# Kernel optimization log

Measured on AMD Instinct MI355X. Metric: run time of the kernel, lower is better.

## Reference

```python
import jax, jax.numpy as jnp
import numpy as np
from jax import lax


def build_scharr_filter(size):
    assert size % 2 == 1
    c = size // 2
    wx = np.zeros((size, size), np.float32)
    wy = np.zeros((size, size), np.float32)
    for i in range(size):
        for j in range(size):
            dx = j - c
            dy = i - c
            wx[i, j] = dx * (3 if abs(dx) == 1 else 10 if dx == 0 else 1)
            wy[i, j] = dy * (3 if abs(dy) == 1 else 10 if dy == 0 else 1)
    return jnp.asarray(wx), jnp.asarray(wy)


SIZE = 3


def build_normals(xyz, size=SIZE):
    # xyz: (B, 3, H, W). Depthwise conv: for each of x,y,z apply scharr_x and scharr_y.
    kx, ky = build_scharr_filter(size)
    # kernel (6,1,s,s): [Sxx, Sxy, Syx, Syy, Szx, Szy] via feature_group_count=3
    kernel = jnp.stack([kx, ky, kx, ky, kx, ky])[:, None]
    p = size // 2
    g = lax.conv_general_dilated(
        xyz, kernel, window_strides=(1, 1), padding=[(p, p), (p, p)],
        dimension_numbers=("NCHW", "OIHW", "NCHW"), feature_group_count=3)
    Sxx, Sxy = g[:, 0:1], g[:, 1:2]
    Syx, Syy = g[:, 2:3], g[:, 3:4]
    Szx, Szy = g[:, 4:5], g[:, 5:6]
    normal = jnp.concatenate([
        Syx * Szy - Szx * Syy,
        Szx * Sxy - Szy * Sxx,
        Sxx * Syy - Syx * Sxy,
    ], axis=1)
    n = jnp.linalg.norm(normal, axis=1, keepdims=True) + jnp.float32(1e-10)
    return normal / n


def setup_inputs() -> dict:
    key = jax.random.key(0)
    k1, k2, k3 = jax.random.split(key, 3)
    B, H, W = 16, 384, 1280
    xyz_pred = jax.random.normal(k1, (B, 3, H, W), dtype=jnp.float32)
    xyz_gt = jax.random.normal(k2, (B, 3, H, W), dtype=jnp.float32)
    mask = jax.random.uniform(k3, (B, 1, H, W), dtype=jnp.float32)
    return {"xyz_pred": xyz_pred, "xyz_gt": xyz_gt, "mask": mask}


def reference(xyz_pred, xyz_gt, mask):
    normals_pred = build_normals(xyz_pred)
    normals_gt = build_normals(xyz_gt)
    loss = jnp.sum(mask * jnp.abs(normals_pred - normals_gt))
    denom = jnp.sum(mask)
    return loss / denom
```

## Files before the change

### kernel.cpp

```cpp
#include <hip/hip_runtime.h>

#define BB  16
#define HH  384
#define WW  1280
#define ROWS 16
#define CPW 62
#define NGROUP 21
#define NSLOT 64


__device__ __forceinline__ float load_col(const float* __restrict__ plane,
                                          int i, int j, bool jok) {
    return jok ? plane[(size_t)i * WW + j] : 0.f;
}

__device__ __forceinline__ void taps(float v, float& D, float& T) {
    const float lft = __shfl_up(v, 1, 64);
    const float rgt = __shfl_down(v, 1, 64);
    D = rgt - lft;
    T = lft + v + rgt;
}

__device__ __forceinline__ float normal_absdiff(const float* gx, const float* gy)
{
    float n0p = gx[1] * gy[2] - gx[2] * gy[1];
    float n1p = gx[2] * gy[0] - gx[0] * gy[2];
    float n2p = gx[0] * gy[1] - gx[1] * gy[0];
    float n0g = gx[4] * gy[5] - gx[5] * gy[4];
    float n1g = gx[5] * gy[3] - gx[3] * gy[5];
    float n2g = gx[3] * gy[4] - gx[4] * gy[3];
    float sp = n0p * n0p + n1p * n1p + n2p * n2p;
    float sg = n0g * n0g + n1g * n1g + n2g * n2g;
    float ip = (sp > 1e-20f) ? __builtin_amdgcn_rsqf(sp) : 0.f;
    float ig = (sg > 1e-20f) ? __builtin_amdgcn_rsqf(sg) : 0.f;
    return fabsf(n0p * ip - n0g * ig) + fabsf(n1p * ip - n1g * ig)
         + fabsf(n2p * ip - n2g * ig);
}

__global__ __launch_bounds__(64)
void NormalLoss_44478681317469_main(const float* __restrict__ pred,
                                    const float* __restrict__ gt,
                                    const float* __restrict__ mask,
                                    double* __restrict__ acc)
{
    const int lane = threadIdx.x;
    const int j    = blockIdx.x * CPW - 1 + lane;
    const bool jok = (unsigned)j < WW;
    const int r0   = blockIdx.y * ROWS;
    const int b    = blockIdx.z;
    const bool out_ok = (lane >= 1) && (lane <= CPW) && jok;

    const float* pl[6];
#pragma unroll
    for (int c = 0; c < 3; ++c) {
        pl[c]     = pred + (size_t)(b * 3 + c) * HH * WW;
        pl[3 + c] = gt   + (size_t)(b * 3 + c) * HH * WW;
    }
    const float* mpl = mask + (size_t)b * HH * WW;

    float Dm1[6], D0[6], Tm1[6], T0[6];
    float Rv[6];

#pragma unroll
    for (int c = 0; c < 6; ++c) {
        if (r0 > 0) {
            float v = load_col(pl[c], r0 - 1, j, jok);
            taps(v, Dm1[c], Tm1[c]);
        } else { Dm1[c] = 0.f; Tm1[c] = 0.f; }
        {
            float v = load_col(pl[c], r0, j, jok);
            taps(v, D0[c], T0[c]);
        }
    }

#pragma unroll
    for (int c = 0; c < 6; ++c)
        Rv[c] = load_col(pl[c], r0 + 1, j, jok);
    float mrow = jok ? mpl[(size_t)r0 * WW + j] : 0.f;

    float lsum = 0.f, msum = 0.f;

#pragma unroll 2
    for (int k = 0; k < ROWS; ++k) {
        const int i = r0 + k;

        float Dp1[6], Tp1[6];
#pragma unroll
        for (int c = 0; c < 6; ++c) taps(Rv[c], Dp1[c], Tp1[c]);
        const float m = out_ok ? mrow : 0.f;

        if (i + 2 < HH) {
#pragma unroll
            for (int c = 0; c < 6; ++c) Rv[c] = load_col(pl[c], i + 2, j, jok);
        } else {
#pragma unroll
            for (int c = 0; c < 6; ++c) Rv[c] = 0.f;
        }
        if (k + 1 < ROWS) mrow = jok ? mpl[(size_t)(i + 1) * WW + j] : 0.f;

        float gx[6], gy[6];
#pragma unroll
        for (int c = 0; c < 6; ++c) {
            gx[c] = Dm1[c] + D0[c] + Dp1[c];
            gy[c] = Tp1[c] - Tm1[c];
        }

        const float d = normal_absdiff(gx, gy);
        lsum += m * d;
        msum += m;

#pragma unroll
        for (int c = 0; c < 6; ++c) {
            Dm1[c] = D0[c]; D0[c] = Dp1[c];
            Tm1[c] = T0[c]; T0[c] = Tp1[c];
        }
    }

#pragma unroll
    for (int off = 32; off > 0; off >>= 1) {
        lsum += __shfl_down(lsum, off, 64);
        msum += __shfl_down(msum, off, 64);
    }
    if (lane == 0) {
        const int linear = (blockIdx.z * gridDim.y + blockIdx.y) * gridDim.x + blockIdx.x;
        double* slot = acc + (size_t)(linear & (NSLOT - 1)) * 8;
        atomicAdd(&slot[0], (double)lsum);
        atomicAdd(&slot[1], (double)msum);
    }
}

__global__ void NormalLoss_44478681317469_final(const double* __restrict__ acc,
                                                float* __restrict__ out)
{
    const int t = threadIdx.x;
    double L = acc[(size_t)t * 8 + 0];
    double M = acc[(size_t)t * 8 + 1];
#pragma unroll
    for (int off = 32; off > 0; off >>= 1) {
        L += __shfl_down(L, off, 64);
        M += __shfl_down(M, off, 64);
    }
    if (t == 0) out[0] = (float)(L / M);
}

extern "C" void kernel_launch(void* const* d_in, const int* in_sizes, int n_in,
                              void* d_out, int out_size, void* d_ws, size_t ws_size,
                              hipStream_t stream)
{
    const float* pred = (const float*)d_in[0];
    const float* gt   = (const float*)d_in[1];
    const float* mask = (const float*)d_in[2];
    double* acc = (double*)d_ws;

    hipMemsetAsync(acc, 0, NSLOT * 8 * sizeof(double), stream);

    dim3 grid(NGROUP, HH / ROWS, BB);
    NormalLoss_44478681317469_main<<<grid, dim3(64), 0, stream>>>(pred, gt, mask, acc);
    NormalLoss_44478681317469_final<<<1, 64, 0, stream>>>(acc, (float*)d_out);
}
```

Baseline: 242.7 us.

## Process two columns per lane with float2 loads and edge halo fetch

Each lane now handles two adjacent columns through float2 loads, so a 64-lane wave covers 128 output columns instead of 62. The old layout wasted two halo lanes per wave; now only the end lanes issue an extra scalar load for the halo. This cuts redundant loads and shuffles per output and widens memory transactions. The cost is roughly double the register state per lane, which may lower occupancy.

```diff
diff --git a/kernel.cpp b/kernel.cpp
--- a/kernel.cpp
+++ b/kernel.cpp
@@ -1,24 +1,32 @@
 #include <hip/hip_runtime.h>
+
 
 #define BB  16
 #define HH  384
 #define WW  1280
 #define ROWS 16
-#define CPW 62
-#define NGROUP 21
+#define CPW 128
 #define NSLOT 64
 
 
-__device__ __forceinline__ float load_col(const float* __restrict__ plane,
-                                          int i, int j, bool jok) {
-    return jok ? plane[(size_t)i * WW + j] : 0.f;
+__device__ __forceinline__ void fetch_pair_edge(const float* __restrict__ plane,
+                                                int i, int x0, int ej, bool eok,
+                                                float& a, float& b, float& e) {
+    const float* row = plane + (size_t)i * WW;
+    const float2 ab = *reinterpret_cast<const float2*>(row + x0);
+    a = ab.x; b = ab.y;
+    e = eok ? row[ej] : 0.f;
 }
 
-__device__ __forceinline__ void taps(float v, float& D, float& T) {
-    const float lft = __shfl_up(v, 1, 64);
-    const float rgt = __shfl_down(v, 1, 64);
-    D = rgt - lft;
-    T = lft + v + rgt;
+__device__ __forceinline__ void htaps(float a, float b, float e, int lane,
+                                      float& Da, float& Db, float& Ta, float& Tb) {
+    float l = __shfl_up(b, 1, 64);
+    float r = __shfl_down(a, 1, 64);
+    if (lane == 0)  l = e;
+    if (lane == 63) r = e;
+    const float s = a + b;
+    Da = b - l;  Db = r - a;
+    Ta = l + s;  Tb = s + r;
 }
 
 __device__ __forceinline__ float normal_absdiff(const float* gx, const float* gy)
@@ -44,11 +52,13 @@
                                     double* __restrict__ acc)
 {
     const int lane = threadIdx.x;
-    const int j    = blockIdx.x * CPW - 1 + lane;
-    const bool jok = (unsigned)j < WW;
+    const int S    = blockIdx.x * CPW;
+    const int x0   = S + 2 * lane;
     const int r0   = blockIdx.y * ROWS;
     const int b    = blockIdx.z;
-    const bool out_ok = (lane >= 1) && (lane <= CPW) && jok;
+
+    const int  ej  = (lane == 0) ? (x0 - 1) : (x0 + 2);
+    const bool eok = ((lane == 0) || (lane == 63)) && ((unsigned)ej < WW);
 
     const float* pl[6];
 #pragma unroll
@@ -58,25 +68,26 @@
     }
     const float* mpl = mask + (size_t)b * HH * WW;
 
-    float Dm1[6], D0[6], Tm1[6], T0[6];
-    float Rv[6];
+    float Dm1a[6], Dm1b[6], D0a[6], D0b[6];
+    float Tm1a[6], Tm1b[6], T0a[6], T0b[6];
+    float Ra[6], Rb[6], Re[6];
 
 #pragma unroll
     for (int c = 0; c < 6; ++c) {
         if (r0 > 0) {
-            float v = load_col(pl[c], r0 - 1, j, jok);
-            taps(v, Dm1[c], Tm1[c]);
-        } else { Dm1[c] = 0.f; Tm1[c] = 0.f; }
+            float a, bb, e; fetch_pair_edge(pl[c], r0 - 1, x0, ej, eok, a, bb, e);
+            htaps(a, bb, e, lane, Dm1a[c], Dm1b[c], Tm1a[c], Tm1b[c]);
+        } else { Dm1a[c] = 0.f; Dm1b[c] = 0.f; Tm1a[c] = 0.f; Tm1b[c] = 0.f; }
         {
-            float v = load_col(pl[c], r0, j, jok);
-            taps(v, D0[c], T0[c]);
+            float a, bb, e; fetch_pair_edge(pl[c], r0, x0, ej, eok, a, bb, e);
+            htaps(a, bb, e, lane, D0a[c], D0b[c], T0a[c], T0b[c]);
         }
     }
 
 #pragma unroll
     for (int c = 0; c < 6; ++c)
-        Rv[c] = load_col(pl[c], r0 + 1, j, jok);
-    float mrow = jok ? mpl[(size_t)r0 * WW + j] : 0.f;
+        fetch_pair_edge(pl[c], r0 + 1, x0, ej, eok, Ra[c], Rb[c], Re[c]);
+    float2 mrow = *reinterpret_cast<const float2*>(mpl + (size_t)r0 * WW + x0);
 
     float lsum = 0.f, msum = 0.f;
 
@@ -84,35 +95,43 @@
     for (int k = 0; k < ROWS; ++k) {
         const int i = r0 + k;
 
-        float Dp1[6], Tp1[6];
+        float Dp1a[6], Dp1b[6], Tp1a[6], Tp1b[6];
 #pragma unroll
-        for (int c = 0; c < 6; ++c) taps(Rv[c], Dp1[c], Tp1[c]);
-        const float m = out_ok ? mrow : 0.f;
+        for (int c = 0; c < 6; ++c)
+            htaps(Ra[c], Rb[c], Re[c], lane, Dp1a[c], Dp1b[c], Tp1a[c], Tp1b[c]);
+        const float2 m = mrow;
 
         if (i + 2 < HH) {
 #pragma unroll
-            for (int c = 0; c < 6; ++c) Rv[c] = load_col(pl[c], i + 2, j, jok);
+            for (int c = 0; c < 6; ++c)
+                fetch_pair_edge(pl[c], i + 2, x0, ej, eok, Ra[c], Rb[c], Re[c]);
         } else {
 #pragma unroll
-            for (int c = 0; c < 6; ++c) Rv[c] = 0.f;
+            for (int c = 0; c < 6; ++c) { Ra[c] = 0.f; Rb[c] = 0.f; Re[c] = 0.f; }
         }
-        if (k + 1 < ROWS) mrow = jok ? mpl[(size_t)(i + 1) * WW + j] : 0.f;
+        if (k + 1 < ROWS)
+            mrow = *reinterpret_cast<const float2*>(mpl + (size_t)(i + 1) * WW + x0);
 
-        float gx[6], gy[6];
+        float gxa[6], gxb[6], gya[6], gyb[6];
 #pragma unroll
         for (int c = 0; c < 6; ++c) {
-            gx[c] = Dm1[c] + D0[c] + Dp1[c];
-            gy[c] = Tp1[c] - Tm1[c];
+            gxa[c] = Dm1a[c] + D0a[c] + Dp1a[c];
+            gxb[c] = Dm1b[c] + D0b[c] + Dp1b[c];
+            gya[c] = Tp1a[c] - Tm1a[c];
+            gyb[c] = Tp1b[c] - Tm1b[c];
         }
 
-        const float d = normal_absdiff(gx, gy);
-        lsum += m * d;
-        msum += m;
+        const float da = normal_absdiff(gxa, gya);
+        const float db = normal_absdiff(gxb, gyb);
+        lsum += m.x * da + m.y * db;
+        msum += m.x + m.y;
 
 #pragma unroll
         for (int c = 0; c < 6; ++c) {
-            Dm1[c] = D0[c]; D0[c] = Dp1[c];
-            Tm1[c] = T0[c]; T0[c] = Tp1[c];
+            Dm1a[c] = D0a[c]; D0a[c] = Dp1a[c];
+            Dm1b[c] = D0b[c]; D0b[c] = Dp1b[c];
+            Tm1a[c] = T0a[c]; T0a[c] = Tp1a[c];
+            Tm1b[c] = T0b[c]; T0b[c] = Tp1b[c];
         }
     }
 
@@ -154,7 +173,7 @@
 
     hipMemsetAsync(acc, 0, NSLOT * 8 * sizeof(double), stream);
 
-    dim3 grid(NGROUP, HH / ROWS, BB);
+    dim3 grid(WW / CPW, HH / ROWS, BB);
     NormalLoss_44478681317469_main<<<grid, dim3(64), 0, stream>>>(pred, gt, mask, acc);
     NormalLoss_44478681317469_final<<<1, 64, 0, stream>>>(acc, (float*)d_out);
 }
```

Measured after the change: 249.7 us. 1.03x slower.

## Process four columns per lane with float4 loads and no halo lanes

Applied to the files above, without the earlier changes.

Each lane now handles four adjacent columns, loaded as one float4, so a 64-lane wave covers 256 columns. Edge lanes fetch one extra scalar halo value instead of a whole wave reserving two halo lanes. This removes the duplicated halo loads and idle lanes, cuts the number of shuffles per output, and widens the memory accesses. It costs more registers for the per-column rolling state and shrinks the grid to five blocks across the width, which lowers parallelism per row band.

```diff
diff --git a/kernel.cpp b/kernel.cpp
--- a/kernel.cpp
+++ b/kernel.cpp
@@ -4,21 +4,26 @@
 #define HH  384
 #define WW  1280
 #define ROWS 16
-#define CPW 62
-#define NGROUP 21
+#define CPW 256
 #define NSLOT 64
 
 
-__device__ __forceinline__ float load_col(const float* __restrict__ plane,
-                                          int i, int j, bool jok) {
-    return jok ? plane[(size_t)i * WW + j] : 0.f;
+__device__ __forceinline__ void load_q(const float* __restrict__ plane, int i, int x0,
+                                       int ej, bool eok, float4& v, float& e) {
+    const float* row = plane + (size_t)i * WW;
+    v = *reinterpret_cast<const float4*>(row + x0);
+    e = eok ? row[ej] : 0.f;
 }
 
-__device__ __forceinline__ void taps(float v, float& D, float& T) {
-    const float lft = __shfl_up(v, 1, 64);
-    const float rgt = __shfl_down(v, 1, 64);
-    D = rgt - lft;
-    T = lft + v + rgt;
+__device__ __forceinline__ void taps4(const float4 v, float e, int lane,
+                                      float D[4], float T[4]) {
+    float l = __shfl_up(v.w, 1, 64);
+    float r = __shfl_down(v.x, 1, 64);
+    if (lane == 0)  l = e;
+    if (lane == 63) r = e;
+    const float s01 = v.x + v.y, s23 = v.z + v.w;
+    D[0] = v.y - l;   D[1] = v.z - v.x;   D[2] = v.w - v.y;   D[3] = r - v.z;
+    T[0] = l + s01;   T[1] = s01 + v.z;   T[2] = v.y + s23;   T[3] = s23 + r;
 }
 
 __device__ __forceinline__ float normal_absdiff(const float* gx, const float* gy)
@@ -44,11 +49,13 @@
                                     double* __restrict__ acc)
 {
     const int lane = threadIdx.x;
-    const int j    = blockIdx.x * CPW - 1 + lane;
-    const bool jok = (unsigned)j < WW;
+    const int S    = blockIdx.x * CPW;
+    const int x0   = S + 4 * lane;
     const int r0   = blockIdx.y * ROWS;
     const int b    = blockIdx.z;
-    const bool out_ok = (lane >= 1) && (lane <= CPW) && jok;
+
+    const int  ej  = (lane == 0) ? (x0 - 1) : (x0 + 4);
+    const bool eok = ((lane == 0) || (lane == 63)) && ((unsigned)ej < WW);
 
     const float* pl[6];
 #pragma unroll
@@ -58,62 +65,75 @@
     }
     const float* mpl = mask + (size_t)b * HH * WW;
 
-    float Dm1[6], D0[6], Tm1[6], T0[6];
-    float Rv[6];
+    float Dm1[6][4], D0[6][4], Tm1[6][4], T0[6][4];
+    float4 Rv[6]; float Re[6];
 
 #pragma unroll
     for (int c = 0; c < 6; ++c) {
         if (r0 > 0) {
-            float v = load_col(pl[c], r0 - 1, j, jok);
-            taps(v, Dm1[c], Tm1[c]);
-        } else { Dm1[c] = 0.f; Tm1[c] = 0.f; }
+            float4 v; float e; load_q(pl[c], r0 - 1, x0, ej, eok, v, e);
+            taps4(v, e, lane, Dm1[c], Tm1[c]);
+        } else {
+#pragma unroll
+            for (int q = 0; q < 4; ++q) { Dm1[c][q] = 0.f; Tm1[c][q] = 0.f; }
+        }
         {
-            float v = load_col(pl[c], r0, j, jok);
-            taps(v, D0[c], T0[c]);
+            float4 v; float e; load_q(pl[c], r0, x0, ej, eok, v, e);
+            taps4(v, e, lane, D0[c], T0[c]);
         }
     }
 
 #pragma unroll
     for (int c = 0; c < 6; ++c)
-        Rv[c] = load_col(pl[c], r0 + 1, j, jok);
-    float mrow = jok ? mpl[(size_t)r0 * WW + j] : 0.f;
+        load_q(pl[c], r0 + 1, x0, ej, eok, Rv[c], Re[c]);
+    float4 mrow = *reinterpret_cast<const float4*>(mpl + (size_t)r0 * WW + x0);
 
     float lsum = 0.f, msum = 0.f;
 
-#pragma unroll 2
     for (int k = 0; k < ROWS; ++k) {
         const int i = r0 + k;
 
-        float Dp1[6], Tp1[6];
+        float lR[6], rR[6];
 #pragma unroll
-        for (int c = 0; c < 6; ++c) taps(Rv[c], Dp1[c], Tp1[c]);
-        const float m = out_ok ? mrow : 0.f;
+        for (int c = 0; c < 6; ++c) {
+            float l = __shfl_up(Rv[c].w, 1, 64);
+            float r = __shfl_down(Rv[c].x, 1, 64);
+            if (lane == 0)  l = Re[c];
+            if (lane == 63) r = Re[c];
+            lR[c] = l; rR[c] = r;
+        }
+        const float4 m = mrow;
+
+#pragma unroll
+        for (int q = 0; q < 4; ++q) {
+            float gx[6], gy[6];
+#pragma unroll
+            for (int c = 0; c < 6; ++c) {
+                const float4 R = Rv[c];
+                float Dp1, Tp1;
+                if (q == 0)      { Dp1 = R.y - lR[c];  Tp1 = lR[c] + R.x + R.y; }
+                else if (q == 1) { Dp1 = R.z - R.x;    Tp1 = R.x + R.y + R.z; }
+                else if (q == 2) { Dp1 = R.w - R.y;    Tp1 = R.y + R.z + R.w; }
+                else             { Dp1 = rR[c] - R.z;  Tp1 = R.z + R.w + rR[c]; }
+                gx[c] = Dm1[c][q] + D0[c][q] + Dp1;
+                gy[c] = Tp1 - Tm1[c][q];
+                Dm1[c][q] = D0[c][q]; D0[c][q] = Dp1;
+                Tm1[c][q] = T0[c][q]; T0[c][q] = Tp1;
+            }
+            const float mq = (q == 0) ? m.x : (q == 1) ? m.y : (q == 2) ? m.z : m.w;
+            lsum += mq * normal_absdiff(gx, gy);
+            msum += mq;
+        }
 
         if (i + 2 < HH) {
 #pragma unroll
-            for (int c = 0; c < 6; ++c) Rv[c] = load_col(pl[c], i + 2, j, jok);
+            for (int c = 0; c < 6; ++c) load_q(pl[c], i + 2, x0, ej, eok, Rv[c], Re[c]);
         } else {
 #pragma unroll
-            for (int c = 0; c < 6; ++c) Rv[c] = 0.f;
+            for (int c = 0; c < 6; ++c) { Rv[c] = make_float4(0.f, 0.f, 0.f, 0.f); Re[c] = 0.f; }
         }
-        if (k + 1 < ROWS) mrow = jok ? mpl[(size_t)(i + 1) * WW + j] : 0.f;
-
-        float gx[6], gy[6];
-#pragma unroll
-        for (int c = 0; c < 6; ++c) {
-            gx[c] = Dm1[c] + D0[c] + Dp1[c];
-            gy[c] = Tp1[c] - Tm1[c];
-        }
-
-        const float d = normal_absdiff(gx, gy);
-        lsum += m * d;
-        msum += m;
-
-#pragma unroll
-        for (int c = 0; c < 6; ++c) {
-            Dm1[c] = D0[c]; D0[c] = Dp1[c];
-            Tm1[c] = T0[c]; T0[c] = Tp1[c];
-        }
+        if (k + 1 < ROWS)
+            mrow = *reinterpret_cast<const float4*>(mpl + (size_t)(i + 1) * WW + x0);
     }
 
 #pragma unroll
@@ -154,7 +174,7 @@
 
     hipMemsetAsync(acc, 0, NSLOT * 8 * sizeof(double), stream);
 
-    dim3 grid(NGROUP, HH / ROWS, BB);
+    dim3 grid(WW / CPW, HH / ROWS, BB);
     NormalLoss_44478681317469_main<<<grid, dim3(64), 0, stream>>>(pred, gt, mask, acc);
     NormalLoss_44478681317469_final<<<1, 64, 0, stream>>>(acc, (float*)d_out);
 }
```

Measured after the change: 244.0 us. No clear change (+0.5%).
